# Kernel tuning notes

Measured on AMD Instinct MI355X. Metric: run time of the kernel, lower is better.

Reference implementation:

```python
import jax, jax.numpy as jnp
import numpy as np

S = 10        # spiking_segment_count
TEMP = 50.0

def setup_inputs() -> dict:
    key = jax.random.key(0)
    ks = jax.random.split(key, 6)
    bs, din, dout = 2048, 1024, 1024
    x = jax.random.normal(ks[0], (bs, din), dtype=jnp.float32)
    t = jax.random.uniform(ks[1], (bs,), dtype=jnp.float32)  # in [0,1) subset of [-1,1]
    scale = 1.0 / np.sqrt(din)
    param_W = jax.random.normal(ks[2], (din, dout * S * 3), dtype=jnp.float32) * scale
    param_b = jax.random.normal(ks[3], (dout * S * 3,), dtype=jnp.float32) * 0.01
    norm_W = jax.random.normal(ks[4], (din, dout), dtype=jnp.float32) * scale
    norm_b = jax.random.normal(ks[5], (dout,), dtype=jnp.float32) * 0.01
    return {"x": x, "t": t, "param_W": param_W, "param_b": param_b,
            "norm_W": norm_W, "norm_b": norm_b}

def reference(x, t, param_W, param_b, norm_W, norm_b):
    bs = x.shape[0]
    dout = norm_W.shape[1]
    # param GEMM -> (bs, S, dout, 3)
    params = (x @ param_W + param_b).reshape(bs, S, dout, 3)
    weights = jax.nn.softmax(params[..., 0], axis=1)                 # (bs, S, dout)
    keypoints = jnp.concatenate(
        [jnp.zeros_like(weights[:, :1]), jnp.cumsum(weights, axis=1)], axis=1
    ) * 2.0 - 1.0                                                    # (bs, S+1, dout)
    slopes = jnp.tanh(params[..., 1])
    intercepts = params[..., 2]
    tt = t.reshape(-1, 1, 1)                                         # (bs, 1, 1)
    starts = keypoints[:, :S]
    ends = keypoints[:, 1:]
    residual = slopes * tt + intercepts                              # (bs, S, dout)
    validity = ((tt >= starts) & (tt < ends)) | ((tt == 1.0) & (ends == 1.0))
    vf = validity.astype(x.dtype)
    left_margin = jnp.sum((tt - starts) * vf, axis=1)                # (bs, dout)
    right_margin = jnp.sum((ends - tt) * vf, axis=1)
    lw = jax.nn.sigmoid(-TEMP * left_margin)
    rw = jax.nn.sigmoid(-TEMP * right_margin)
    lv = jnp.concatenate([vf[:, :1], vf[:, :-1]], axis=1)
    rv = jnp.concatenate([vf[:, 1:], vf[:, -1:]], axis=1)
    sw = -(lw + rw - 1.0)
    result = (lw * jnp.sum(residual * lv, axis=1)
              + sw * jnp.sum(residual * vf, axis=1)
              + rw * jnp.sum(residual * rv, axis=1))
    # norm == 'constant': subtract segment-wise integral, add norm_net(x)
    integral = jnp.sum(0.5 * slopes * (ends * ends - starts * starts)
                       + intercepts * weights, axis=1) * 0.5
    norm_target = x @ norm_W + norm_b
    return result - integral + norm_target
```

## Files before the change

### kernel.cpp

```cpp
#include <hip/hip_runtime.h>
#include <cstdint>
#include <cstddef>

#define BS    2048
#define DIN   1024
#define DOUT  1024
#define SSEG  10
#define NPAR  30720
#define NPK   20480
#define NCOL2 21504
#define NLG   10240
#define NT_LG 80
#define NT_SM 168
#define MT    16
#define TAU   5e-5f
#define WL_CAP 1048576u

#define NB_SPLIT 2048
#define NB_NORM  1024
#define NB_TRW   2560

typedef _Float16 half_t;
typedef __attribute__((ext_vector_type(8))) _Float16 half8;
typedef __attribute__((ext_vector_type(4))) _Float16 half4;
typedef __attribute__((ext_vector_type(2))) _Float16 half2v;
typedef __attribute__((ext_vector_type(4))) float   floatx4;

__device__ __forceinline__ void gload16(const void* g, void* l) {
  __builtin_amdgcn_global_load_lds(
      (const __attribute__((address_space(1))) void*)g,
      (__attribute__((address_space(3))) void*)l, 16, 0, 0);
}

__global__ void k_zero(unsigned* c) { if (threadIdx.x == 0) *c = 0; }

__global__ __launch_bounds__(256) void k_prep(const float* __restrict__ x,
                                              half_t* __restrict__ xh,
                                              half_t* __restrict__ xl,
                                              const float* __restrict__ nW,
                                              const float* __restrict__ pW,
                                              half_t* __restrict__ wsm,
                                              half_t* __restrict__ wh,
                                              half_t* __restrict__ wlo,
                                              float* __restrict__ wlt,
                                              unsigned* __restrict__ cnt) {
  __shared__ float tile[32][384];
  int bid = blockIdx.x;
  int tid = threadIdx.x;

  if (bid < NB_SPLIT) {
    if (bid == 0 && tid == 0) *cnt = 0;
    int i = bid * 256 + tid;
    floatx4 v = ((const floatx4*)x)[i];
    half4 h, l;
    #pragma unroll
    for (int c = 0; c < 4; c++) { h[c] = (half_t)v[c]; l[c] = (half_t)(v[c] - (float)h[c]); }
    ((half4*)xh)[i] = h;
    ((half4*)xl)[i] = l;
    return;
  }

  if (bid < NB_SPLIT + NB_NORM) {
    int b2 = bid - NB_SPLIT;
    int col0 = (b2 & 31) * 32;
    int k0   = (b2 >> 5) * 32;
    int tx = tid & 31;
    int ty = tid >> 5;
    float* t33 = &tile[0][0];
    #pragma unroll
    for (int r = ty; r < 32; r += 8)
      t33[r * 33 + tx] = nW[(size_t)(k0 + r) * DOUT + col0 + tx];
    __syncthreads();
    #pragma unroll
    for (int r = ty; r < 32; r += 8)
      wsm[(size_t)(col0 + r + NPK) * DIN + k0 + tx] = (half_t)t33[tx * 33 + r];
    return;
  }

  int b3 = bid - NB_SPLIT - NB_NORM;
  int bx = b3 % 80;
  int k0 = (b3 / 80) * 32;
  int s  = bx >> 3;
  int d0 = (bx & 7) * 128;

  const float* sb = pW + (size_t)k0 * NPAR + bx * 384;
  for (int i = tid; i < 32 * 96; i += 256) {
    int r = i / 96, q = i - r * 96;
    ((floatx4*)&tile[r][0])[q] = ((const floatx4*)(sb + (size_t)r * NPAR))[q];
  }
  __syncthreads();

  for (int ci = tid; ci < 3072; ci += 256) {
    if (ci < 1024) {
      int rl = ci >> 2, kc = ci & 3;
      int jj = rl >> 1, cbit = rl & 1;
      int col = 3 * jj + 1 + cbit;
      half8 v;
      #pragma unroll
      for (int m = 0; m < 8; m++) v[m] = (half_t)tile[kc * 8 + m][col];
      *(half8*)(wsm + (size_t)(s * 2048 + 2 * (d0 + jj) + cbit) * DIN + k0 + kc * 8) = v;
    } else if (ci < 1536) {
      int u = ci - 1024;
      int jj = u >> 2, kc = u & 3;
      half8 v;
      #pragma unroll
      for (int m = 0; m < 8; m++) v[m] = (half_t)(tile[kc * 8 + m][3 * jj] * 32.0f);
      *(half8*)(wh + (size_t)(s * 1024 + d0 + jj) * DIN + k0 + kc * 8) = v;
    } else if (ci < 2048) {
      int u = ci - 1536;
      int jj = u >> 2, kc = u & 3;
      half8 v;
      #pragma unroll
      for (int m = 0; m < 8; m++) {
        float raw = tile[kc * 8 + m][3 * jj] * 32.0f;
        half_t h = (half_t)raw;
        v[m] = (half_t)(raw - (float)h);
      }
      *(half8*)(wlo + (size_t)(s * 1024 + d0 + jj) * DIN + k0 + kc * 8) = v;
    } else {
      int u = ci - 2048;
      int jj = u >> 3, kc = u & 7;
      floatx4 v;
      #pragma unroll
      for (int m = 0; m < 4; m++) v[m] = tile[kc * 4 + m][3 * jj];
      *(floatx4*)(wlt + (size_t)(s * 1024 + d0 + jj) * DIN + k0 + kc * 4) = v;
    }
  }
}

__global__ __launch_bounds__(256) void k_gemm_logit(const half_t* __restrict__ Ah,
                                                    const half_t* __restrict__ Al,
                                                    const half_t* __restrict__ Bh,
                                                    const half_t* __restrict__ Bl,
                                                    float* __restrict__ Lg,
                                                    const float* __restrict__ pb) {
  __shared__ __attribute__((aligned(16))) half_t sAh[128 * 32];
  __shared__ __attribute__((aligned(16))) half_t sAl[128 * 32];
  __shared__ __attribute__((aligned(16))) half_t sBh[128 * 32];
  __shared__ __attribute__((aligned(16))) half_t sBl[128 * 32];
  const int K = DIN;
  int m0 = blockIdx.y * 128, n0 = blockIdx.x * 128;
  int tid = threadIdx.x, w = tid >> 6, L = tid & 63;
  int wm = (w >> 1) * 64, wn = (w & 1) * 64;
  int l15 = L & 15, quad = L >> 4;

  size_t arow = (size_t)(m0 + w * 16 + (L >> 2)) * K + (L & 3) * 8;
  size_t brow = (size_t)(n0 + w * 16 + (L >> 2)) * K + (L & 3) * 8;
  char* lah = (char*)sAh + w * 1024;
  char* lal = (char*)sAl + w * 1024;
  char* lbh = (char*)sBh + w * 1024;
  char* lbl = (char*)sBl + w * 1024;

  floatx4 acc[4][4] = {};

  for (int k0 = 0; k0 < K; k0 += 32) {
    __syncthreads();
    gload16(Ah + arow + k0,          lah);
    gload16(Ah + arow + 64 * K + k0, lah + 4096);
    gload16(Al + arow + k0,          lal);
    gload16(Al + arow + 64 * K + k0, lal + 4096);
    gload16(Bh + brow + k0,          lbh);
    gload16(Bh + brow + 64 * K + k0, lbh + 4096);
    gload16(Bl + brow + k0,          lbl);
    gload16(Bl + brow + 64 * K + k0, lbl + 4096);
    __syncthreads();

    #pragma unroll
    for (int mi = 0; mi < 4; mi++) {
      half8 afh = *(const half8*)((const char*)sAh + (wm + mi * 16 + l15) * 64 + quad * 16);
      half8 afl = *(const half8*)((const char*)sAl + (wm + mi * 16 + l15) * 64 + quad * 16);
      #pragma unroll
      for (int ni = 0; ni < 4; ni++) {
        half8 bfh = *(const half8*)((const char*)sBh + (wn + ni * 16 + l15) * 64 + quad * 16);
        half8 bfl = *(const half8*)((const char*)sBl + (wn + ni * 16 + l15) * 64 + quad * 16);
        floatx4 a = acc[mi][ni];
        a = __builtin_amdgcn_mfma_f32_16x16x32_f16(afh, bfh, a, 0, 0, 0);
        a = __builtin_amdgcn_mfma_f32_16x16x32_f16(afl, bfh, a, 0, 0, 0);
        a = __builtin_amdgcn_mfma_f32_16x16x32_f16(afh, bfl, a, 0, 0, 0);
        acc[mi][ni] = a;
      }
    }
  }

  #pragma unroll
  for (int ni = 0; ni < 4; ni++) {
    int col = n0 + wn + ni * 16 + l15;
    float bias = pb[(col >> 10) * 3072 + (col & 1023) * 3];
    #pragma unroll
    for (int mi = 0; mi < 4; mi++) {
      int row = m0 + wm + mi * 16 + quad * 4;
      floatx4 v = acc[mi][ni];
      #pragma unroll
      for (int r = 0; r < 4; r++)
        Lg[(size_t)(row + r) * NLG + col] = v[r] * 0.03125f + bias;
    }
  }
}

__global__ __launch_bounds__(256) void k_gemm_sm(const half_t* __restrict__ A,
                                                 const half_t* __restrict__ B,
                                                 half_t* __restrict__ P,
                                                 const float* __restrict__ pb,
                                                 const float* __restrict__ nb) {
  __shared__ __attribute__((aligned(16))) half_t As[128 * 32];
  __shared__ __attribute__((aligned(16))) half_t Bs[128 * 32];
  const int K = DIN;
  int m0 = blockIdx.y * 128, n0 = blockIdx.x * 128;
  int tid = threadIdx.x, w = tid >> 6, L = tid & 63;
  int wm = (w >> 1) * 64, wn = (w & 1) * 64;
  int l15 = L & 15, quad = L >> 4;

  const half_t* ga = A + (size_t)(m0 + w * 16 + (L >> 2)) * K + (L & 3) * 8;
  const half_t* gb = B + (size_t)(n0 + w * 16 + (L >> 2)) * K + (L & 3) * 8;
  char* lA = (char*)As + w * 1024;
  char* lB = (char*)Bs + w * 1024;

  floatx4 acc[4][4] = {};

  for (int k0 = 0; k0 < K; k0 += 32) {
    __syncthreads();
    gload16(ga + k0,          lA);
    gload16(ga + 64 * K + k0, lA + 4096);
    gload16(gb + k0,          lB);
    gload16(gb + 64 * K + k0, lB + 4096);
    __syncthreads();

    half8 af[4], bf[4];
    #pragma unroll
    for (int mi = 0; mi < 4; mi++)
      af[mi] = *(const half8*)((const char*)As + (wm + mi * 16 + l15) * 64 + quad * 16);
    #pragma unroll
    for (int ni = 0; ni < 4; ni++)
      bf[ni] = *(const half8*)((const char*)Bs + (wn + ni * 16 + l15) * 64 + quad * 16);
    #pragma unroll
    for (int mi = 0; mi < 4; mi++)
      #pragma unroll
      for (int ni = 0; ni < 4; ni++)
        acc[mi][ni] = __builtin_amdgcn_mfma_f32_16x16x32_f16(af[mi], bf[ni], acc[mi][ni], 0, 0, 0);
  }

  #pragma unroll
  for (int ni = 0; ni < 4; ni++) {
    int col = n0 + wn + ni * 16 + l15;
    float bias;
    if (col < NPK) {
      int s = col >> 11, rem = col & 2047;
      bias = pb[s * 3072 + 3 * (rem >> 1) + 1 + (rem & 1)];
    } else {
      bias = nb[col - NPK];
    }
    #pragma unroll
    for (int mi = 0; mi < 4; mi++) {
      int row = m0 + wm + mi * 16 + quad * 4;
      floatx4 v = acc[mi][ni];
      #pragma unroll
      for (int r = 0; r < 4; r++)
        P[(size_t)(row + r) * NCOL2 + col] = (half_t)(v[r] + bias);
    }
  }
}

__device__ __forceinline__ float spiking_eval(const float* p, float tt, float* mind) {
  float mx = -1e30f;
  #pragma unroll
  for (int s = 0; s < SSEG; s++) mx = fmaxf(mx, p[3 * s]);
  float ew[10], wsum = 0.0f;
  #pragma unroll
  for (int s = 0; s < SSEG; s++) { ew[s] = __expf(p[3 * s] - mx); wsum += ew[s]; }
  float inv = 1.0f / wsum;

  float kp[11];
  kp[0] = -1.0f;
  float cum = 0.0f, md = 1e30f;
  #pragma unroll
  for (int s = 0; s < SSEG; s++) {
    cum += ew[s] * inv;
    kp[s + 1] = cum * 2.0f - 1.0f;
    md = fminf(md, fabsf(tt - kp[s + 1]));
  }
  *mind = md;

  float vf[10], resid[10];
  float lm = 0.0f, rm = 0.0f, integ = 0.0f;
  #pragma unroll
  for (int s = 0; s < SSEG; s++) {
    float p1 = p[3 * s + 1], p2 = p[3 * s + 2];
    float e2 = __expf(2.0f * fabsf(p1));
    float th = copysignf(1.0f - 2.0f / (e2 + 1.0f), p1);
    resid[s] = th * tt + p2;
    float st = kp[s], en = kp[s + 1];
    bool v = ((tt >= st) && (tt < en)) || ((tt == 1.0f) && (en == 1.0f));
    float vv = v ? 1.0f : 0.0f;
    vf[s] = vv;
    lm += (tt - st) * vv;
    rm += (en - tt) * vv;
    integ += 0.5f * th * (en * en - st * st) + p2 * (ew[s] * inv);
  }
  float resLV = 0.0f, resV = 0.0f, resRV = 0.0f;
  #pragma unroll
  for (int s = 0; s < SSEG; s++) {
    float lv = (s == 0) ? vf[0] : vf[s - 1];
    float rv = (s == 9) ? vf[9] : vf[s + 1];
    resLV += resid[s] * lv;
    resV  += resid[s] * vf[s];
    resRV += resid[s] * rv;
  }
  float lw = 1.0f / (1.0f + __expf(50.0f * lm));
  float rw = 1.0f / (1.0f + __expf(50.0f * rm));
  float swt = 1.0f - lw - rw;
  return lw * resLV + swt * resV + rw * resRV - 0.5f * integ + p[30];
}

__global__ __launch_bounds__(256) void k_pointwise(const half_t* __restrict__ P,
                                                   const float* __restrict__ Lg,
                                                   const float* __restrict__ t,
                                                   float* __restrict__ out,
                                                   unsigned* __restrict__ cnt,
                                                   unsigned* __restrict__ wl,
                                                   unsigned cap) {
  __shared__ __attribute__((aligned(16))) half_t sp[SSEG * 512];
  int b = blockIdx.x, dg = blockIdx.y, tid = threadIdx.x;
  const half_t* Pb = P + (size_t)b * NCOL2;
  for (int i = tid; i < SSEG * 64; i += 256) {
    int s = i >> 6, e = i & 63;
    ((uint4*)sp)[(s << 6) + e] = ((const uint4*)(Pb + s * 2048 + dg * 512))[e];
  }
  float tt = t[b];
  float nt = (float)Pb[NPK + dg * 256 + tid];
  const float* Lb = Lg + (size_t)b * NLG + dg * 256 + tid;
  __syncthreads();

  float p[31];
  #pragma unroll
  for (int s = 0; s < SSEG; s++) {
    p[3 * s] = Lb[s * 1024];
    half2v hv = ((const half2v*)sp)[s * 256 + tid];
    p[3 * s + 1] = (float)hv.x;
    p[3 * s + 2] = (float)hv.y;
  }
  p[30] = nt;
  float mind;
  float r = spiking_eval(p, tt, &mind);
  int d = dg * 256 + tid;
  out[(size_t)b * DOUT + d] = r;
  if (wl != nullptr && mind < TAU) {
    unsigned idx = atomicAdd(cnt, 1u);
    if (idx < cap) wl[idx] = ((unsigned)b << 10) | (unsigned)d;
  }
}

__global__ __launch_bounds__(256) void k_naive(const float* __restrict__ x,
                                               const float* __restrict__ t,
                                               const float* __restrict__ pW,
                                               const float* __restrict__ pb,
                                               const float* __restrict__ nW,
                                               const float* __restrict__ nb,
                                               float* __restrict__ out,
                                               unsigned* __restrict__ cnt,
                                               unsigned* __restrict__ wl,
                                               unsigned cap) {
  __shared__ float xs[DIN];
  int b = blockIdx.x, dg = blockIdx.y, tid = threadIdx.x;
  for (int i = tid; i < DIN; i += 256) xs[i] = x[(size_t)b * DIN + i];
  __syncthreads();
  int d = dg * 256 + tid;
  float acc[31];
  #pragma unroll
  for (int i = 0; i < 31; i++) acc[i] = 0.0f;
  for (int k = 0; k < DIN; k++) {
    float xv = xs[k];
    const float* wr = pW + (size_t)k * NPAR + 3 * d;
    #pragma unroll
    for (int s = 0; s < SSEG; s++) {
      acc[3 * s]     += xv * wr[s * 3072];
      acc[3 * s + 1] += xv * wr[s * 3072 + 1];
      acc[3 * s + 2] += xv * wr[s * 3072 + 2];
    }
    acc[30] += xv * nW[(size_t)k * DOUT + d];
  }
  #pragma unroll
  for (int s = 0; s < SSEG; s++) {
    acc[3 * s]     += pb[s * 3072 + 3 * d];
    acc[3 * s + 1] += pb[s * 3072 + 3 * d + 1];
    acc[3 * s + 2] += pb[s * 3072 + 3 * d + 2];
  }
  acc[30] += nb[d];
  float mind;
  float r = spiking_eval(acc, t[b], &mind);
  out[(size_t)b * DOUT + d] = r;
  if (wl != nullptr && mind < TAU) {
    unsigned idx = atomicAdd(cnt, 1u);
    if (idx < cap) wl[idx] = ((unsigned)b << 10) | (unsigned)d;
  }
}

__global__ __launch_bounds__(256) void k_redo(const float* __restrict__ x,
                                              const float* __restrict__ t,
                                              const float* __restrict__ pW,
                                              const float* __restrict__ pb,
                                              const float* __restrict__ nW,
                                              const float* __restrict__ nb,
                                              const half_t* __restrict__ P,
                                              const float* __restrict__ WLt,
                                              int haveP,
                                              const unsigned* __restrict__ cnt,
                                              const unsigned* __restrict__ wl,
                                              unsigned cap,
                                              float* __restrict__ out) {
  unsigned n = *cnt;
  if (n > cap) n = cap;
  int lane = threadIdx.x & 63;
  unsigned wave = (blockIdx.x * 256 + threadIdx.x) >> 6;
  unsigned nwaves = (gridDim.x * 256) >> 6;

  for (unsigned e = wave; e < n; e += nwaves) {
    unsigned code = wl[e];
    int b = (int)(code >> 10), d = (int)(code & 1023);

    double lg[10], sl[10], ic[10], nt = 0.0;
    #pragma unroll
    for (int s = 0; s < SSEG; s++) { lg[s] = 0.0; sl[s] = 0.0; ic[s] = 0.0; }

    if (haveP) {
      for (int k = lane; k < DIN; k += 64) {
        double xv = (double)x[(size_t)b * DIN + k];
        #pragma unroll
        for (int s = 0; s < SSEG; s++)
          lg[s] += xv * (double)WLt[(size_t)(s * 1024 + d) * DIN + k];
      }
    } else {
      for (int k = lane; k < DIN; k += 64) {
        double xv = (double)x[(size_t)b * DIN + k];
        const float* wr = pW + (size_t)k * NPAR + 3 * d;
        #pragma unroll
        for (int s = 0; s < SSEG; s++) {
          lg[s] += xv * (double)wr[s * 3072];
          sl[s] += xv * (double)wr[s * 3072 + 1];
          ic[s] += xv * (double)wr[s * 3072 + 2];
        }
        nt += xv * (double)nW[(size_t)k * DOUT + d];
      }
    }
    #pragma unroll
    for (int off = 32; off > 0; off >>= 1) {
      #pragma unroll
      for (int s = 0; s < SSEG; s++) lg[s] += __shfl_down(lg[s], off);
      if (!haveP) {
        #pragma unroll
        for (int s = 0; s < SSEG; s++) {
          sl[s] += __shfl_down(sl[s], off);
          ic[s] += __shfl_down(ic[s], off);
        }
        nt += __shfl_down(nt, off);
      }
    }

    if (lane == 0) {
      double slope[10], icpt[10], ntv;
      if (haveP) {
        const half_t* Pr = P + (size_t)b * NCOL2;
        #pragma unroll
        for (int s = 0; s < SSEG; s++) {
          slope[s] = tanh((double)(float)Pr[s * 2048 + 2 * d]);
          icpt[s]  = (double)(float)Pr[s * 2048 + 2 * d + 1];
        }
        ntv = (double)(float)Pr[NPK + d];
      } else {
        #pragma unroll
        for (int s = 0; s < SSEG; s++) {
          slope[s] = tanh(sl[s] + (double)pb[s * 3072 + 3 * d + 1]);
          icpt[s]  = ic[s] + (double)pb[s * 3072 + 3 * d + 2];
        }
        ntv = nt + (double)nb[d];
      }
      #pragma unroll
      for (int s = 0; s < SSEG; s++) lg[s] += (double)pb[s * 3072 + 3 * d];

      double mx = -1e300;
      #pragma unroll
      for (int s = 0; s < SSEG; s++) mx = fmax(mx, lg[s]);
      double ew[10], ws = 0.0;
      #pragma unroll
      for (int s = 0; s < SSEG; s++) { ew[s] = exp(lg[s] - mx); ws += ew[s]; }

      double kp[11];
      kp[0] = -1.0;
      double cum = 0.0;
      #pragma unroll
      for (int s = 0; s < SSEG; s++) { cum += ew[s] / ws; kp[s + 1] = cum * 2.0 - 1.0; }

      double tt = (double)t[b];
      double vf[10], resid[10], lm = 0.0, rm = 0.0, integ = 0.0;
      #pragma unroll
      for (int s = 0; s < SSEG; s++) {
        double st = kp[s], en = kp[s + 1];
        bool v = ((tt >= st) && (tt < en)) || ((tt == 1.0) && (en == 1.0));
        double vv = v ? 1.0 : 0.0;
        vf[s] = vv;
        resid[s] = slope[s] * tt + icpt[s];
        lm += (tt - st) * vv;
        rm += (en - tt) * vv;
        integ += 0.5 * slope[s] * (en * en - st * st) + icpt[s] * (ew[s] / ws);
      }
      double rLV = 0.0, rV = 0.0, rRV = 0.0;
      #pragma unroll
      for (int s = 0; s < SSEG; s++) {
        double lv = (s == 0) ? vf[0] : vf[s - 1];
        double rv = (s == 9) ? vf[9] : vf[s + 1];
        rLV += resid[s] * lv;
        rV  += resid[s] * vf[s];
        rRV += resid[s] * rv;
      }
      double lw = 1.0 / (1.0 + exp(50.0 * lm));
      double rw = 1.0 / (1.0 + exp(50.0 * rm));
      double res = lw * rLV + (1.0 - lw - rw) * rV + rw * rRV - 0.5 * integ + ntv;
      out[(size_t)b * DOUT + d] = (float)res;
    }
  }
}

extern "C" void kernel_launch(void* const* d_in, const int* in_sizes, int n_in,
                              void* d_out, int out_size, void* d_ws, size_t ws_size,
                              hipStream_t stream) {
  const float* x  = (const float*)d_in[0];
  const float* t  = (const float*)d_in[1];
  const float* pW = (const float*)d_in[2];
  const float* pb = (const float*)d_in[3];
  const float* nW = (const float*)d_in[4];
  const float* nb = (const float*)d_in[5];
  float* out = (float*)d_out;

  const size_t o_cnt = 0;
  const size_t o_wl  = 64;
  const size_t o_xh  = o_wl  + (size_t)WL_CAP * 4;
  const size_t o_xl  = o_xh  + (size_t)BS * DIN * 2;
  const size_t o_wsm = o_xl  + (size_t)BS * DIN * 2;
  const size_t o_wh  = o_wsm + (size_t)NCOL2 * DIN * 2;
  const size_t o_wlo = o_wh  + (size_t)NLG * DIN * 2;
  const size_t o_wlt = o_wlo + (size_t)NLG * DIN * 2;
  const size_t o_p   = o_wlt + (size_t)NLG * DIN * 4;
  const size_t o_lg  = o_p   + (size_t)BS * NCOL2 * 2;
  const size_t need  = o_lg  + (size_t)BS * NLG * 4;

  bool have_wl = ws_size >= 1024 * 1024;
  unsigned* cnt = (unsigned*)((char*)d_ws + o_cnt);
  unsigned* wl  = (unsigned*)((char*)d_ws + o_wl);
  unsigned cap  = 0;
  if (have_wl) {
    size_t avail = (ws_size >= need) ? (size_t)WL_CAP
                                     : (ws_size - o_wl) / 4;
    cap = (unsigned)(avail < WL_CAP ? avail : WL_CAP);
  }

  if (ws_size >= need) {
    half_t* xh  = (half_t*)((char*)d_ws + o_xh);
    half_t* xl  = (half_t*)((char*)d_ws + o_xl);
    half_t* wsm = (half_t*)((char*)d_ws + o_wsm);
    half_t* wh  = (half_t*)((char*)d_ws + o_wh);
    half_t* wlo = (half_t*)((char*)d_ws + o_wlo);
    float*  wlt = (float*)((char*)d_ws + o_wlt);
    half_t* P   = (half_t*)((char*)d_ws + o_p);
    float*  Lg  = (float*)((char*)d_ws + o_lg);

    k_prep<<<NB_SPLIT + NB_NORM + NB_TRW, 256, 0, stream>>>(x, xh, xl, nW, pW,
                                                            wsm, wh, wlo, wlt, cnt);
    k_gemm_logit<<<dim3(NT_LG, MT), 256, 0, stream>>>(xh, xl, wh, wlo, Lg, pb);
    k_gemm_sm<<<dim3(NT_SM, MT), 256, 0, stream>>>(xh, wsm, P, pb, nb);
    k_pointwise<<<dim3(BS, DOUT / 256), 256, 0, stream>>>(P, Lg, t, out, cnt,
                                                          have_wl ? wl : nullptr, cap);
    if (have_wl)
      k_redo<<<256, 256, 0, stream>>>(x, t, pW, pb, nW, nb, P, wlt, 1, cnt, wl, cap, out);
  } else {
    if (have_wl) k_zero<<<1, 64, 0, stream>>>(cnt);
    k_naive<<<dim3(BS, DOUT / 256), 256, 0, stream>>>(x, t, pW, pb, nW, nb, out, cnt,
                                                      have_wl ? wl : nullptr, cap);
    if (have_wl)
      k_redo<<<256, 256, 0, stream>>>(x, t, pW, pb, nW, nb, nullptr, nullptr, 0,
                                      cnt, wl, cap, out);
  }
}
```

Measured before the change: 574.7 us.

## Merge logit and param GEMMs into one pipelined 256x256-tile kernel

```diff
diff --git a/kernel.cpp b/kernel.cpp
--- a/kernel.cpp
+++ b/kernel.cpp
@@ -10,15 +10,14 @@
 #define NPK   20480
 #define NCOL2 21504
 #define NLG   10240
-#define NT_LG 80
-#define NT_SM 168
-#define MT    16
 #define TAU   5e-5f
 #define WL_CAP 1048576u
 
 #define NB_SPLIT 2048
 #define NB_NORM  1024
 #define NB_TRW   2560
+
+#define GEMM_BLKS 992
 
 typedef _Float16 half_t;
 typedef __attribute__((ext_vector_type(8))) _Float16 half8;
@@ -128,134 +127,141 @@
   }
 }
 
-__global__ __launch_bounds__(256) void k_gemm_logit(const half_t* __restrict__ Ah,
-                                                    const half_t* __restrict__ Al,
-                                                    const half_t* __restrict__ Bh,
-                                                    const half_t* __restrict__ Bl,
-                                                    float* __restrict__ Lg,
-                                                    const float* __restrict__ pb) {
-  __shared__ __attribute__((aligned(16))) half_t sAh[128 * 32];
-  __shared__ __attribute__((aligned(16))) half_t sAl[128 * 32];
-  __shared__ __attribute__((aligned(16))) half_t sBh[128 * 32];
-  __shared__ __attribute__((aligned(16))) half_t sBl[128 * 32];
-  const int K = DIN;
-  int m0 = blockIdx.y * 128, n0 = blockIdx.x * 128;
-  int tid = threadIdx.x, w = tid >> 6, L = tid & 63;
-  int wm = (w >> 1) * 64, wn = (w & 1) * 64;
-  int l15 = L & 15, quad = L >> 4;
-
-  size_t arow = (size_t)(m0 + w * 16 + (L >> 2)) * K + (L & 3) * 8;
-  size_t brow = (size_t)(n0 + w * 16 + (L >> 2)) * K + (L & 3) * 8;
-  char* lah = (char*)sAh + w * 1024;
-  char* lal = (char*)sAl + w * 1024;
-  char* lbh = (char*)sBh + w * 1024;
-  char* lbl = (char*)sBl + w * 1024;
-
-  floatx4 acc[4][4] = {};
-
-  for (int k0 = 0; k0 < K; k0 += 32) {
-    __syncthreads();
-    gload16(Ah + arow + k0,          lah);
-    gload16(Ah + arow + 64 * K + k0, lah + 4096);
-    gload16(Al + arow + k0,          lal);
-    gload16(Al + arow + 64 * K + k0, lal + 4096);
-    gload16(Bh + brow + k0,          lbh);
-    gload16(Bh + brow + 64 * K + k0, lbh + 4096);
-    gload16(Bl + brow + k0,          lbl);
-    gload16(Bl + brow + 64 * K + k0, lbl + 4096);
-    __syncthreads();
-
-    #pragma unroll
-    for (int mi = 0; mi < 4; mi++) {
-      half8 afh = *(const half8*)((const char*)sAh + (wm + mi * 16 + l15) * 64 + quad * 16);
-      half8 afl = *(const half8*)((const char*)sAl + (wm + mi * 16 + l15) * 64 + quad * 16);
-      #pragma unroll
-      for (int ni = 0; ni < 4; ni++) {
-        half8 bfh = *(const half8*)((const char*)sBh + (wn + ni * 16 + l15) * 64 + quad * 16);
-        half8 bfl = *(const half8*)((const char*)sBl + (wn + ni * 16 + l15) * 64 + quad * 16);
-        floatx4 a = acc[mi][ni];
-        a = __builtin_amdgcn_mfma_f32_16x16x32_f16(afh, bfh, a, 0, 0, 0);
-        a = __builtin_amdgcn_mfma_f32_16x16x32_f16(afl, bfh, a, 0, 0, 0);
-        a = __builtin_amdgcn_mfma_f32_16x16x32_f16(afh, bfl, a, 0, 0, 0);
-        acc[mi][ni] = a;
-      }
-    }
-  }
-
-  #pragma unroll
-  for (int ni = 0; ni < 4; ni++) {
-    int col = n0 + wn + ni * 16 + l15;
-    float bias = pb[(col >> 10) * 3072 + (col & 1023) * 3];
-    #pragma unroll
-    for (int mi = 0; mi < 4; mi++) {
-      int row = m0 + wm + mi * 16 + quad * 4;
-      floatx4 v = acc[mi][ni];
-      #pragma unroll
-      for (int r = 0; r < 4; r++)
-        Lg[(size_t)(row + r) * NLG + col] = v[r] * 0.03125f + bias;
-    }
-  }
-}
-
-__global__ __launch_bounds__(256) void k_gemm_sm(const half_t* __restrict__ A,
-                                                 const half_t* __restrict__ B,
-                                                 half_t* __restrict__ P,
-                                                 const float* __restrict__ pb,
-                                                 const float* __restrict__ nb) {
-  __shared__ __attribute__((aligned(16))) half_t As[128 * 32];
-  __shared__ __attribute__((aligned(16))) half_t Bs[128 * 32];
-  const int K = DIN;
-  int m0 = blockIdx.y * 128, n0 = blockIdx.x * 128;
-  int tid = threadIdx.x, w = tid >> 6, L = tid & 63;
-  int wm = (w >> 1) * 64, wn = (w & 1) * 64;
-  int l15 = L & 15, quad = L >> 4;
-
-  const half_t* ga = A + (size_t)(m0 + w * 16 + (L >> 2)) * K + (L & 3) * 8;
-  const half_t* gb = B + (size_t)(n0 + w * 16 + (L >> 2)) * K + (L & 3) * 8;
-  char* lA = (char*)As + w * 1024;
-  char* lB = (char*)Bs + w * 1024;
-
-  floatx4 acc[4][4] = {};
-
-  for (int k0 = 0; k0 < K; k0 += 32) {
-    __syncthreads();
-    gload16(ga + k0,          lA);
-    gload16(ga + 64 * K + k0, lA + 4096);
-    gload16(gb + k0,          lB);
-    gload16(gb + 64 * K + k0, lB + 4096);
-    __syncthreads();
-
+__global__ __launch_bounds__(512, 2) void k_gemm2(
+    const half_t* __restrict__ xh, const half_t* __restrict__ xl,
+    const half_t* __restrict__ wh, const half_t* __restrict__ wlo,
+    const half_t* __restrict__ wsm,
+    float* __restrict__ Lg, half_t* __restrict__ P,
+    const float* __restrict__ pb, const float* __restrict__ nb) {
+  __shared__ __attribute__((aligned(128))) char lds[131072];
+  char* ldsA = lds;
+  char* ldsB = lds + 65536;
+
+  int bid = blockIdx.x;
+  int tid = threadIdx.x;
+  int w = tid >> 6, l = tid & 63;
+  int wr = w >> 2, wc = w & 3;
+  int l15 = l & 15, quad = l >> 4;
+
+  int mode, mt, nt, KT;
+  const half_t *A0, *A1, *A2, *B0, *B1, *B2;
+  if (bid < 320) {
+    int s = (bid & 7) * 40 + (bid >> 3);
+    mode = 0; mt = s & 7; nt = s >> 3; KT = 96;
+    A0 = xh; A1 = xl; A2 = xh; B0 = wh; B1 = wh; B2 = wlo;
+  } else {
+    int s2 = bid - 320;
+    int s = (s2 & 7) * 84 + (s2 >> 3);
+    mode = 1; mt = s & 7; nt = s >> 3; KT = 32;
+    A0 = xh; A1 = xh; A2 = xh; B0 = wsm; B1 = wsm; B2 = wsm;
+  }
+  int m0 = mt * 256, n0 = nt * 256;
+
+  int sp = (l & 7) ^ ((l >> 3) & 7);
+  int srowA = m0 + w * 32 + 2 * (l >> 3) + (sp >> 2);
+  int srowB = n0 + w * 32 + 2 * (l >> 3) + (sp >> 2);
+  int scol = (sp & 3) * 8;
+
+  int lofs = (l15 >> 1) * 128 + (((((l15 & 1) << 2) | quad) ^ (l15 >> 1)) << 4);
+  const char* pA = ldsA + wr * 8192 + lofs;
+  const char* pB = ldsB + wc * 4096 + lofs;
+
+  auto stA = [&](int kt) {
+    const half_t* As = (kt < 32) ? A0 : ((kt < 64) ? A1 : A2);
+    const half_t* g = As + (size_t)srowA * DIN + (kt & 31) * 32 + scol;
+    char* lb = ldsA + (kt & 3) * 16384 + w * 2048;
+    gload16(g, lb);
+    gload16(g + 16 * DIN, lb + 1024);
+  };
+  auto stB = [&](int kt) {
+    const half_t* Bs = (kt < 32) ? B0 : ((kt < 64) ? B1 : B2);
+    const half_t* g = Bs + (size_t)srowB * DIN + (kt & 31) * 32 + scol;
+    char* lb = ldsB + (kt & 3) * 16384 + w * 2048;
+    gload16(g, lb);
+    gload16(g + 16 * DIN, lb + 1024);
+  };
+
+  floatx4 acc[8][4] = {};
+
+  stA(0); stB(0); stA(1); stB(1); stA(2); stB(2);
+  asm volatile("s_waitcnt vmcnt(8)" ::: "memory");
+  __builtin_amdgcn_s_barrier();
+
+  for (int kt = 0; kt < KT; ++kt) {
+    const char* a = pA + (kt & 3) * 16384;
+    const char* b = pB + (kt & 3) * 16384;
     half8 af[4], bf[4];
     #pragma unroll
-    for (int mi = 0; mi < 4; mi++)
-      af[mi] = *(const half8*)((const char*)As + (wm + mi * 16 + l15) * 64 + quad * 16);
-    #pragma unroll
-    for (int ni = 0; ni < 4; ni++)
-      bf[ni] = *(const half8*)((const char*)Bs + (wn + ni * 16 + l15) * 64 + quad * 16);
+    for (int ni = 0; ni < 4; ni++) bf[ni] = *(const half8*)(b + ni * 1024);
+    #pragma unroll
+    for (int mi = 0; mi < 4; mi++) af[mi] = *(const half8*)(a + mi * 1024);
+    if (kt + 3 < KT) stA(kt + 3);
+    __builtin_amdgcn_s_barrier();
+    asm volatile("s_waitcnt lgkmcnt(0)" ::: "memory");
+    __builtin_amdgcn_sched_barrier(0);
+    __builtin_amdgcn_s_setprio(1);
     #pragma unroll
     for (int mi = 0; mi < 4; mi++)
       #pragma unroll
       for (int ni = 0; ni < 4; ni++)
         acc[mi][ni] = __builtin_amdgcn_mfma_f32_16x16x32_f16(af[mi], bf[ni], acc[mi][ni], 0, 0, 0);
-  }
-
-  #pragma unroll
-  for (int ni = 0; ni < 4; ni++) {
-    int col = n0 + wn + ni * 16 + l15;
-    float bias;
-    if (col < NPK) {
-      int s = col >> 11, rem = col & 2047;
-      bias = pb[s * 3072 + 3 * (rem >> 1) + 1 + (rem & 1)];
-    } else {
-      bias = nb[col - NPK];
-    }
-    #pragma unroll
-    for (int mi = 0; mi < 4; mi++) {
-      int row = m0 + wm + mi * 16 + quad * 4;
-      floatx4 v = acc[mi][ni];
-      #pragma unroll
-      for (int r = 0; r < 4; r++)
-        P[(size_t)(row + r) * NCOL2 + col] = (half_t)(v[r] + bias);
+    __builtin_amdgcn_s_setprio(0);
+    __builtin_amdgcn_s_barrier();
+
+    #pragma unroll
+    for (int mi = 0; mi < 4; mi++) af[mi] = *(const half8*)(a + 4096 + mi * 1024);
+    if (kt + 3 < KT) stB(kt + 3);
+    __builtin_amdgcn_s_barrier();
+    asm volatile("s_waitcnt lgkmcnt(0)" ::: "memory");
+    __builtin_amdgcn_sched_barrier(0);
+    __builtin_amdgcn_s_setprio(1);
+    #pragma unroll
+    for (int mi = 0; mi < 4; mi++)
+      #pragma unroll
+      for (int ni = 0; ni < 4; ni++)
+        acc[4 + mi][ni] = __builtin_amdgcn_mfma_f32_16x16x32_f16(af[mi], bf[ni], acc[4 + mi][ni], 0, 0, 0);
+    __builtin_amdgcn_s_setprio(0);
+    if (kt < KT - 3)       { asm volatile("s_waitcnt vmcnt(8)" ::: "memory"); }
+    else if (kt == KT - 3) { asm volatile("s_waitcnt vmcnt(4)" ::: "memory"); }
+    else if (kt == KT - 2) { asm volatile("s_waitcnt vmcnt(0)" ::: "memory"); }
+    __builtin_amdgcn_s_barrier();
+  }
+
+  int rbase = m0 + wr * 128 + quad * 4;
+  int cbase = n0 + wc * 64 + l15;
+  if (mode == 0) {
+    #pragma unroll
+    for (int ni = 0; ni < 4; ni++) {
+      int col = cbase + ni * 16;
+      float bias = pb[(col >> 10) * 3072 + (col & 1023) * 3];
+      #pragma unroll
+      for (int mi = 0; mi < 8; mi++) {
+        int row = rbase + mi * 16;
+        floatx4 v = acc[mi][ni];
+        #pragma unroll
+        for (int r = 0; r < 4; r++)
+          Lg[(size_t)(row + r) * NLG + col] = v[r] * 0.03125f + bias;
+      }
+    }
+  } else {
+    #pragma unroll
+    for (int ni = 0; ni < 4; ni++) {
+      int col = cbase + ni * 16;
+      float bias;
+      if (col < NPK) {
+        int s = col >> 11, rem = col & 2047;
+        bias = pb[s * 3072 + 3 * (rem >> 1) + 1 + (rem & 1)];
+      } else {
+        bias = nb[col - NPK];
+      }
+      #pragma unroll
+      for (int mi = 0; mi < 8; mi++) {
+        int row = rbase + mi * 16;
+        floatx4 v = acc[mi][ni];
+        #pragma unroll
+        for (int r = 0; r < 4; r++)
+          P[(size_t)(row + r) * NCOL2 + col] = (half_t)(v[r] + bias);
+      }
     }
   }
 }
@@ -564,8 +570,7 @@
 
     k_prep<<<NB_SPLIT + NB_NORM + NB_TRW, 256, 0, stream>>>(x, xh, xl, nW, pW,
                                                             wsm, wh, wlo, wlt, cnt);
-    k_gemm_logit<<<dim3(NT_LG, MT), 256, 0, stream>>>(xh, xl, wh, wlo, Lg, pb);
-    k_gemm_sm<<<dim3(NT_SM, MT), 256, 0, stream>>>(xh, wsm, P, pb, nb);
+    k_gemm2<<<GEMM_BLKS, 512, 0, stream>>>(xh, xl, wh, wlo, wsm, Lg, P, pb, nb);
     k_pointwise<<<dim3(BS, DOUT / 256), 256, 0, stream>>>(P, Lg, t, out, cnt,
                                                           have_wl ? wl : nullptr, cap);
     if (have_wl)
```

Result: faster. 561.2 us (-2.3%).
